# Kernel optimization log

Measured on AMD Instinct MI355X. Metric: run time of the kernel, lower is better.

The kernel has to match this reference:

```python
import jax, jax.numpy as jnp
import numpy as np

DEPTH = 4
HEADS = 8
DIM_HEAD = 32
NUM_CLUSTERS = 64
KMEANS_ITERS = 10
EPS = 1e-5


def layer_norm(x, g, b):
    m = jnp.mean(x, axis=-1, keepdims=True)
    v = jnp.var(x, axis=-1, keepdims=True)
    return (x - m) * jax.lax.rsqrt(v + EPS) * g + b


def kmeans_cluster(xf, k, iters):
    # xf: [P, D]. Lloyd's algorithm with deterministic init (first k points).
    centers = xf[:k]
    x_sq = jnp.sum(xf * xf, axis=-1, keepdims=True)  # [P,1]

    def assign(c):
        # squared distances [P, K]
        d = x_sq - 2.0 * (xf @ c.T) + jnp.sum(c * c, axis=-1)[None, :]
        return jnp.argmin(d, axis=-1)

    def step(c, _):
        labels = assign(c)
        sums = jax.ops.segment_sum(xf, labels, num_segments=k)
        counts = jax.ops.segment_sum(jnp.ones((xf.shape[0],), xf.dtype), labels, num_segments=k)
        new_c = jnp.where(counts[:, None] > 0, sums / jnp.maximum(counts, 1.0)[:, None], c)
        return new_c, None

    centers, _ = jax.lax.scan(step, centers, None, length=iters)
    labels = assign(centers)
    return centers[labels]  # gather: [P, D]


def setup_inputs() -> dict:
    key = jax.random.key(0)
    ks = jax.random.split(key, 8)
    B, N, D, L, M = 8, 1024, 256, DEPTH, 1024
    s = 0.02
    return {
        "x": jax.random.normal(ks[0], (B, N, D), jnp.float32),
        "ln1_g": jnp.ones((L, D), jnp.float32),
        "ln1_b": jnp.zeros((L, D), jnp.float32),
        "Wq": jax.random.normal(ks[1], (L, D, HEADS * DIM_HEAD), jnp.float32) * s,
        "Wkv": jax.random.normal(ks[2], (L, D, 2 * HEADS * DIM_HEAD), jnp.float32) * s,
        "Wo": jax.random.normal(ks[3], (L, HEADS * DIM_HEAD, D), jnp.float32) * s,
        "bo": jnp.zeros((L, D), jnp.float32),
        "ln2_g": jnp.ones((L, D), jnp.float32),
        "ln2_b": jnp.zeros((L, D), jnp.float32),
        "W1": jax.random.normal(ks[4], (L, D, M), jnp.float32) * s,
        "b1": jnp.zeros((L, M), jnp.float32),
        "W2": jax.random.normal(ks[5], (L, M, D), jnp.float32) * s,
        "b2": jnp.zeros((L, D), jnp.float32),
        "kW": jax.random.normal(ks[6], (D, D), jnp.float32) * s,
        "kb": jnp.zeros((D,), jnp.float32),
    }


def reference(x, ln1_g, ln1_b, Wq, Wkv, Wo, bo, ln2_g, ln2_b, W1, b1, W2, b2, kW, kb):
    B, N, D = x.shape
    h, dh = HEADS, DIM_HEAD
    scale = dh ** -0.5
    for l in range(DEPTH):
        # PreNorm self-attention + residual
        xn = layer_norm(x, ln1_g[l], ln1_b[l])
        q = (xn @ Wq[l]).reshape(B, N, h, dh)
        kv = xn @ Wkv[l]
        k, v = jnp.split(kv, 2, axis=-1)
        k = k.reshape(B, N, h, dh)
        v = v.reshape(B, N, h, dh)
        dots = jnp.einsum("bqhd,bkhd->bhqk", q, k) * scale
        attn = jax.nn.softmax(dots, axis=-1)
        out = jnp.einsum("bhqk,bkhd->bqhd", attn, v).reshape(B, N, h * dh)
        x = out @ Wo[l] + bo[l] + x
        # PreNorm FFN + residual
        xn = layer_norm(x, ln2_g[l], ln2_b[l])
        hdd = jax.nn.gelu(xn @ W1[l] + b1[l], approximate=False)
        x = hdd @ W2[l] + b2[l] + x
    # KMeans module: cluster flattened tokens, gather centers, linear transform.
    xf = x.reshape(B * N, D)
    clustered = kmeans_cluster(xf, NUM_CLUSTERS, KMEANS_ITERS)
    clustered = jax.lax.stop_gradient(clustered)  # torch detaches before sklearn
    clustered = clustered.reshape(B, N, D)
    return clustered @ kW + kb
```

## Files before the change

### kernel.cpp

```cpp
#include <hip/hip_runtime.h>
#include <hip/hip_bf16.h>
#include <math.h>

#define BN 8192
#define DMODEL 256
#define FFN 1024
#define NCLUST 64

typedef unsigned short u16;
typedef unsigned int u32;
typedef __attribute__((ext_vector_type(8))) short s16x8;
typedef __attribute__((ext_vector_type(8))) unsigned short u16x8;
typedef __attribute__((ext_vector_type(4))) unsigned short u16x4;
typedef __attribute__((ext_vector_type(4))) float f32x4;

__device__ __forceinline__ float bf2f(u16 v) {
    union { unsigned int u; float f; } w; w.u = ((unsigned int)v) << 16; return w.f;
}
__device__ __forceinline__ u16 f2bf(float f) {
    union { float f; unsigned int u; } w; w.f = f;
    unsigned int r = w.u + 0x7fffu + ((w.u >> 16) & 1u);
    return (u16)(r >> 16);
}

__device__ __forceinline__ void gl16(const u16* g, u16* l) {
    __builtin_amdgcn_global_load_lds((const __attribute__((address_space(1))) u32*)g,
                                     (__attribute__((address_space(3))) u32*)l, 16, 0, 0);
}

#define BARRIER_LGKM() asm volatile("s_waitcnt lgkmcnt(0)\n\ts_barrier" ::: "memory")
#define MEMFENCE_ORDER() asm volatile("" ::: "memory")

__device__ __forceinline__ int sw32(int row, int col) { return row * 32 + (col ^ (((row >> 1) & 3) << 3)); }
__device__ __forceinline__ int sw64(int row, int col) { return row * 64 + (col ^ ((row & 7) << 3)); }

__global__ __launch_bounds__(256) void ln_wave(const float* __restrict__ x, const float* __restrict__ g,
                                               const float* __restrict__ b, u16* __restrict__ yh,
                                               u16* __restrict__ yl) {
    int t = threadIdx.x, w = t >> 6, l = t & 63;
    int row = blockIdx.x * 4 + w;
    const float* xr = x + (size_t)row * DMODEL;
    float4 v = *reinterpret_cast<const float4*>(xr + l * 4);
    float s = v.x + v.y + v.z + v.w;
    for (int off = 1; off < 64; off <<= 1) s += __shfl_xor(s, off);
    float mean = s * (1.0f / 256.0f);
    float4 dv = make_float4(v.x - mean, v.y - mean, v.z - mean, v.w - mean);
    float vs = dv.x * dv.x + dv.y * dv.y + dv.z * dv.z + dv.w * dv.w;
    for (int off = 1; off < 64; off <<= 1) vs += __shfl_xor(vs, off);
    float rs = rsqrtf(vs * (1.0f / 256.0f) + 1e-5f);
    float4 gg = *reinterpret_cast<const float4*>(g + l * 4);
    float4 bb = *reinterpret_cast<const float4*>(b + l * 4);
    float os[4] = {dv.x * rs * gg.x + bb.x, dv.y * rs * gg.y + bb.y,
                   dv.z * rs * gg.z + bb.z, dv.w * rs * gg.w + bb.w};
    u16x4 hv, lv;
#pragma unroll
    for (int j = 0; j < 4; j++) { u16 hh = f2bf(os[j]); hv[j] = hh; lv[j] = f2bf(os[j] - bf2f(hh)); }
    size_t o = (size_t)row * DMODEL + l * 4;
    *reinterpret_cast<u16x4*>(yh + o) = hv;
    *reinterpret_cast<u16x4*>(yl + o) = lv;
}

__device__ __forceinline__ void wconv_body(const float* __restrict__ W, u16* __restrict__ th,
                                           u16* __restrict__ tl, int K, int N, int bx, int by) {
    __shared__ float T[64][65];
    int k0 = by * 64, n0 = bx * 64;
    int t = threadIdx.x;
    int r = t >> 4, c4 = (t & 15) * 4;
#pragma unroll
    for (int i = 0; i < 4; i++) {
        float4 x = *reinterpret_cast<const float4*>(W + (size_t)(k0 + r + 16 * i) * N + n0 + c4);
        T[r + 16 * i][c4] = x.x; T[r + 16 * i][c4 + 1] = x.y;
        T[r + 16 * i][c4 + 2] = x.z; T[r + 16 * i][c4 + 3] = x.w;
    }
    __syncthreads();
#pragma unroll
    for (int i = 0; i < 4; i++) {
        int n = r + 16 * i;
        u16x4 h4, l4;
#pragma unroll
        for (int j = 0; j < 4; j++) {
            float v = T[c4 + j][n];
            u16 h = f2bf(v);
            h4[j] = h; l4[j] = f2bf(v - bf2f(h));
        }
        *reinterpret_cast<u16x4*>(th + (size_t)(n0 + n) * K + k0 + c4) = h4;
        *reinterpret_cast<u16x4*>(tl + (size_t)(n0 + n) * K + k0 + c4) = l4;
    }
}

__global__ __launch_bounds__(256) void wconv_all(const float* __restrict__ Wq, const float* __restrict__ Wkv,
                                                 const float* __restrict__ Wo, const float* __restrict__ W1,
                                                 const float* __restrict__ W2,
                                                 u16* __restrict__ wqkvh, u16* __restrict__ wqkvl,
                                                 u16* __restrict__ woh, u16* __restrict__ wol,
                                                 u16* __restrict__ w1h, u16* __restrict__ w1l,
                                                 u16* __restrict__ w2h, u16* __restrict__ w2l) {
    int f = blockIdx.x;
    if (f < 16)       wconv_body(Wq,  wqkvh,               wqkvl,               256, 256,  f & 3,  f >> 2);
    else if (f < 48)  { int g = f - 16;  wconv_body(Wkv, wqkvh + 65536,       wqkvl + 65536,       256, 512,  g & 7,  g >> 3); }
    else if (f < 64)  { int g = f - 48;  wconv_body(Wo,  woh,                 wol,                 256, 256,  g & 3,  g >> 2); }
    else if (f < 128) { int g = f - 64;  wconv_body(W1,  w1h,                 w1l,                 256, 1024, g & 15, g >> 4); }
    else              { int g = f - 128; wconv_body(W2,  w2h,                 w2l,                 1024, 256, g & 3,  g >> 2); }
}

template<int BM, int BNT>
__global__ __launch_bounds__(256) void gemm_t(const u16* __restrict__ Ath, const u16* __restrict__ Atl,
                                              const u16* __restrict__ Bth, const u16* __restrict__ Btl,
                                              const float* __restrict__ bias, const float* __restrict__ resid,
                                              float* __restrict__ Cf, u16* __restrict__ Ch, u16* __restrict__ Cl,
                                              int M, int N, int K, int fuse_gelu) {
    __shared__ u16 Ah[2][BM * 32], Al[2][BM * 32];
    __shared__ u16 Bh[2][BNT * 32], Bl[2][BNT * 32];
    constexpr int WAVES_N = (BM == 128 && BNT == 64) ? 1 : 2;
    constexpr int WAVES_M = 4 / WAVES_N;
    constexpr int MI = BM / (16 * WAVES_M);
    constexpr int NI = BNT / (16 * WAVES_N);
    constexpr int SEGS = (BM + BNT) / 32;
    constexpr int ASEG = BM / 16, BSEG = BNT / 16;
    int t = threadIdx.x;
    int m0 = blockIdx.y * BM, n0 = blockIdx.x * BNT;
    int L = t & 63, w = t >> 6, fr = L & 15, quad = L >> 4;
    int wm = (WAVES_N == 1) ? w : (w & 1);
    int wn = (WAVES_N == 1) ? 0 : (w >> 1);

    const u16* gsrc[SEGS];
    u16* ldst[SEGS];
    u32 dlt[SEGS];
    {
        int lr = L >> 2, lc = (L & 3) * 8;
#pragma unroll
        for (int i = 0; i < SEGS; i++) {
            int s = w * SEGS + i;
            const u16* gb; u16* lb; int r; u32 d;
            if (s < ASEG)                 { gb = Ath + (size_t)m0 * K; lb = &Ah[0][0]; r = s * 16;                 d = BM * 32; }
            else if (s < 2 * ASEG)        { gb = Atl + (size_t)m0 * K; lb = &Al[0][0]; r = (s - ASEG) * 16;        d = BM * 32; }
            else if (s < 2 * ASEG + BSEG) { gb = Bth + (size_t)n0 * K; lb = &Bh[0][0]; r = (s - 2 * ASEG) * 16;    d = BNT * 32; }
            else                          { gb = Btl + (size_t)n0 * K; lb = &Bl[0][0]; r = (s - 2 * ASEG - BSEG) * 16; d = BNT * 32; }
            int row = r + lr;
            int scol = lc ^ (((row >> 1) & 3) << 3);
            gsrc[i] = gb + (size_t)row * K + scol;
            ldst[i] = lb + r * 32;
            dlt[i] = d;
        }
    }

    f32x4 acc[MI][NI];
#pragma unroll
    for (int i = 0; i < MI; i++)
#pragma unroll
        for (int j = 0; j < NI; j++) acc[i][j] = (f32x4){0.0f, 0.0f, 0.0f, 0.0f};

    const int NT = K >> 5;
#pragma unroll
    for (int i = 0; i < SEGS; i++) gl16(gsrc[i], ldst[i]);

    for (int tt = 0; tt < NT; tt++) {
        asm volatile("s_waitcnt lgkmcnt(0)" ::: "memory");
        __builtin_amdgcn_s_barrier();
        if (tt + 1 < NT) {
            int k0n = (tt + 1) * 32;
            u32 sel = (u32)((tt + 1) & 1);
#pragma unroll
            for (int i = 0; i < SEGS; i++) gl16(gsrc[i] + k0n, ldst[i] + sel * dlt[i]);
            asm volatile("s_waitcnt vmcnt(%0)" :: "n"(SEGS) : "memory");
        } else {
            asm volatile("s_waitcnt vmcnt(0)" ::: "memory");
        }
        __builtin_amdgcn_s_barrier();
        __builtin_amdgcn_sched_barrier(0);
        int cb = tt & 1;
        const u16* AhB = &Ah[cb][0]; const u16* AlB = &Al[cb][0];
        const u16* BhB = &Bh[cb][0]; const u16* BlB = &Bl[cb][0];
        s16x8 ah[MI], al[MI];
#pragma unroll
        for (int mi = 0; mi < MI; mi++) {
            int row = wm * (MI * 16) + mi * 16 + fr;
            ah[mi] = *reinterpret_cast<const s16x8*>(&AhB[sw32(row, quad * 8)]);
            al[mi] = *reinterpret_cast<const s16x8*>(&AlB[sw32(row, quad * 8)]);
        }
        __builtin_amdgcn_s_setprio(1);
#pragma unroll
        for (int ni = 0; ni < NI; ni++) {
            int rn = wn * (NI * 16) + ni * 16 + fr;
            s16x8 bhf = *reinterpret_cast<const s16x8*>(&BhB[sw32(rn, quad * 8)]);
            s16x8 blf = *reinterpret_cast<const s16x8*>(&BlB[sw32(rn, quad * 8)]);
#pragma unroll
            for (int mi = 0; mi < MI; mi++) {
                acc[mi][ni] = __builtin_amdgcn_mfma_f32_16x16x32_bf16(ah[mi], bhf, acc[mi][ni], 0, 0, 0);
                acc[mi][ni] = __builtin_amdgcn_mfma_f32_16x16x32_bf16(ah[mi], blf, acc[mi][ni], 0, 0, 0);
                acc[mi][ni] = __builtin_amdgcn_mfma_f32_16x16x32_bf16(al[mi], bhf, acc[mi][ni], 0, 0, 0);
            }
        }
        __builtin_amdgcn_s_setprio(0);
    }
#pragma unroll
    for (int mi = 0; mi < MI; mi++) {
#pragma unroll
        for (int ni = 0; ni < NI; ni++) {
#pragma unroll
            for (int r = 0; r < 4; r++) {
                int row = m0 + wm * (MI * 16) + mi * 16 + quad * 4 + r;
                int col = n0 + wn * (NI * 16) + ni * 16 + fr;
                float v = acc[mi][ni][r];
                if (bias) v += bias[col];
                if (fuse_gelu) v = 0.5f * v * (1.0f + erff(v * 0.70710678118654752f));
                if (resid) v += resid[(size_t)row * N + col];
                size_t o = (size_t)row * N + col;
                if (Cf) Cf[o] = v;
                if (Ch) { u16 hh = f2bf(v); Ch[o] = hh; Cl[o] = f2bf(v - bf2f(hh)); }
            }
        }
    }
}

__global__ __launch_bounds__(256) void attn12(const u16* __restrict__ qkvh, const u16* __restrict__ qkvl,
                                              u16* __restrict__ aoh, u16* __restrict__ aol) {
    int bh = blockIdx.x, b = bh >> 3, h = bh & 7;
    int qt = blockIdx.y;
    int t = threadIdx.x, L = t & 63, w = t >> 6;
    int fr = L & 15, quad = L >> 4;
    __shared__ u16 KH[2][64 * 32], KL[2][64 * 32];
    __shared__ u16 VTH[32 * 64], VTL[32 * 64];
    __shared__ u16 PH[4][16 * 64], PL[4][16 * 64];
    const float scale = 0.17677669529663687f;
    const int ROWS = 768;

    const u16* ksrc[2];
    u16* kdst[2];
    {
        int lr = L >> 2, lc = (L & 3) * 8;
#pragma unroll
        for (int i = 0; i < 2; i++) {
            int s = w * 2 + i;
            const u16* gb = (s < 4) ? qkvh : qkvl;
            u16* lb = (s < 4) ? &KH[0][0] : &KL[0][0];
            int r = (s & 3) * 16;
            int row = r + lr;
            int scol = lc ^ (((row >> 1) & 3) << 3);
            ksrc[i] = gb + ((size_t)(b * 1024) + row) * ROWS + 256 + h * 32 + scol;
            kdst[i] = lb + r * 32;
        }
    }

    size_t qoff = (size_t)(b * 1024 + qt * 64 + w * 16 + fr) * ROWS + h * 32 + quad * 8;
    s16x8 aqh = *reinterpret_cast<const s16x8*>(qkvh + qoff);
    s16x8 aql = *reinterpret_cast<const s16x8*>(qkvl + qoff);

    int vp = t >> 3, vd0 = (t & 7) * 4;
    const u16* vh_ptr = qkvh + (size_t)(b * 1024 + 2 * vp) * ROWS + 512 + h * 32 + vd0;
    const u16* vl_ptr = qkvl + (size_t)(b * 1024 + 2 * vp) * ROWS + 512 + h * 32 + vd0;
    u16x4 vh0, vh1, vl0, vl1;
#define LOADV(kt_) do { size_t o_ = (size_t)((kt_) * 64) * ROWS;                                  \
        vh0 = *reinterpret_cast<const u16x4*>(vh_ptr + o_);                                       \
        vh1 = *reinterpret_cast<const u16x4*>(vh_ptr + o_ + ROWS);                                \
        vl0 = *reinterpret_cast<const u16x4*>(vl_ptr + o_);                                       \
        vl1 = *reinterpret_cast<const u16x4*>(vl_ptr + o_ + ROWS); } while (0)

    gl16(ksrc[0], kdst[0]);
    gl16(ksrc[1], kdst[1]);
    MEMFENCE_ORDER();
    LOADV(0);

    float m_i = -1e30f, l_i = 0.0f;
    f32x4 acc_o[2];
    acc_o[0] = (f32x4){0.0f, 0.0f, 0.0f, 0.0f};
    acc_o[1] = (f32x4){0.0f, 0.0f, 0.0f, 0.0f};

#pragma unroll 2
    for (int kt = 0; kt < 16; kt++) {
        int cur = kt & 1;
        BARRIER_LGKM();
        if (kt < 15) {
            size_t koff = (size_t)((kt + 1) * 64) * ROWS;
            u32 sel = (u32)((kt + 1) & 1) * (64 * 32);
            gl16(ksrc[0] + koff, kdst[0] + sel);
            gl16(ksrc[1] + koff, kdst[1] + sel);
        }
        {
#pragma unroll
            for (int i = 0; i < 4; i++) {
                int idx = sw64(vd0 + i, 2 * vp);
                *reinterpret_cast<u32*>(&VTH[idx]) = (u32)vh0[i] | ((u32)vh1[i] << 16);
                *reinterpret_cast<u32*>(&VTL[idx]) = (u32)vl0[i] | ((u32)vl1[i] << 16);
            }
        }
        BARRIER_LGKM();
        f32x4 sv[4];
        __builtin_amdgcn_s_setprio(1);
#pragma unroll
        for (int ni = 0; ni < 4; ni++) {
            s16x8 bkh = *reinterpret_cast<s16x8*>(&KH[cur][sw32(ni * 16 + fr, quad * 8)]);
            s16x8 bkl = *reinterpret_cast<s16x8*>(&KL[cur][sw32(ni * 16 + fr, quad * 8)]);
            f32x4 c = (f32x4){0.0f, 0.0f, 0.0f, 0.0f};
            c = __builtin_amdgcn_mfma_f32_16x16x32_bf16(bkh, aqh, c, 0, 0, 0);
            c = __builtin_amdgcn_mfma_f32_16x16x32_bf16(bkl, aqh, c, 0, 0, 0);
            c = __builtin_amdgcn_mfma_f32_16x16x32_bf16(bkh, aql, c, 0, 0, 0);
            sv[ni] = c;
        }
        __builtin_amdgcn_s_setprio(0);
        if (kt < 15) LOADV(kt + 1);
        float p[16];
        float ml = -1e30f;
#pragma unroll
        for (int ni = 0; ni < 4; ni++)
#pragma unroll
            for (int r = 0; r < 4; r++) { float v = sv[ni][r] * scale; p[ni * 4 + r] = v; ml = fmaxf(ml, v); }
        ml = fmaxf(ml, __shfl_xor(ml, 16));
        ml = fmaxf(ml, __shfl_xor(ml, 32));
        float mnew = fmaxf(m_i, ml);
        float alpha = __expf(m_i - mnew);
        m_i = mnew;
        float rs = 0.0f;
#pragma unroll
        for (int i = 0; i < 16; i++) { float e = __expf(p[i] - mnew); p[i] = e; rs += e; }
        rs += __shfl_xor(rs, 16);
        rs += __shfl_xor(rs, 32);
        l_i = l_i * alpha + rs;
#pragma unroll
        for (int ni = 0; ni < 4; ni++) {
            float p0 = p[ni * 4], p1 = p[ni * 4 + 1], p2 = p[ni * 4 + 2], p3 = p[ni * 4 + 3];
            u16 h0 = f2bf(p0), h1 = f2bf(p1), h2 = f2bf(p2), h3 = f2bf(p3);
            u16 e0 = f2bf(p0 - bf2f(h0)), e1 = f2bf(p1 - bf2f(h1));
            u16 e2 = f2bf(p2 - bf2f(h2)), e3 = f2bf(p3 - bf2f(h3));
            int c0 = sw64(fr, ni * 16 + quad * 4);
            int c1 = sw64(fr, ni * 16 + quad * 4 + 2);
            *reinterpret_cast<u32*>(&PH[w][c0]) = (u32)h0 | ((u32)h1 << 16);
            *reinterpret_cast<u32*>(&PH[w][c1]) = (u32)h2 | ((u32)h3 << 16);
            *reinterpret_cast<u32*>(&PL[w][c0]) = (u32)e0 | ((u32)e1 << 16);
            *reinterpret_cast<u32*>(&PL[w][c1]) = (u32)e2 | ((u32)e3 << 16);
        }
        float a4[4];
#pragma unroll
        for (int r = 0; r < 4; r++) a4[r] = __shfl(alpha, quad * 4 + r);
        acc_o[0][0] *= a4[0]; acc_o[0][1] *= a4[1]; acc_o[0][2] *= a4[2]; acc_o[0][3] *= a4[3];
        acc_o[1][0] *= a4[0]; acc_o[1][1] *= a4[1]; acc_o[1][2] *= a4[2]; acc_o[1][3] *= a4[3];
        __builtin_amdgcn_s_setprio(1);
#pragma unroll
        for (int ks = 0; ks < 2; ks++) {
            s16x8 aph = *reinterpret_cast<s16x8*>(&PH[w][sw64(fr, ks * 32 + quad * 8)]);
            s16x8 apl = *reinterpret_cast<s16x8*>(&PL[w][sw64(fr, ks * 32 + quad * 8)]);
#pragma unroll
            for (int ns = 0; ns < 2; ns++) {
                s16x8 bvh = *reinterpret_cast<s16x8*>(&VTH[sw64(ns * 16 + fr, ks * 32 + quad * 8)]);
                s16x8 bvl = *reinterpret_cast<s16x8*>(&VTL[sw64(ns * 16 + fr, ks * 32 + quad * 8)]);
                acc_o[ns] = __builtin_amdgcn_mfma_f32_16x16x32_bf16(aph, bvh, acc_o[ns], 0, 0, 0);
                acc_o[ns] = __builtin_amdgcn_mfma_f32_16x16x32_bf16(aph, bvl, acc_o[ns], 0, 0, 0);
                acc_o[ns] = __builtin_amdgcn_mfma_f32_16x16x32_bf16(apl, bvh, acc_o[ns], 0, 0, 0);
            }
        }
        __builtin_amdgcn_s_setprio(0);
    }
#undef LOADV
    float invl = 1.0f / l_i;
#pragma unroll
    for (int r = 0; r < 4; r++) {
        float iv = __shfl(invl, quad * 4 + r);
        size_t rowbase = ((size_t)(b * 1024 + qt * 64 + w * 16 + quad * 4 + r)) * DMODEL + h * 32;
        float v0 = acc_o[0][r] * iv, v1 = acc_o[1][r] * iv;
        u16 h0 = f2bf(v0); aoh[rowbase + fr] = h0;      aol[rowbase + fr] = f2bf(v0 - bf2f(h0));
        u16 h1 = f2bf(v1); aoh[rowbase + 16 + fr] = h1; aol[rowbase + 16 + fr] = f2bf(v1 - bf2f(h1));
    }
}

__global__ __launch_bounds__(64) void csq_k(const float* __restrict__ centers, float* __restrict__ csq) {
    int j = blockIdx.x, l = threadIdx.x;
    float4 c4 = *reinterpret_cast<const float4*>(centers + j * DMODEL + l * 4);
    float s = c4.x * c4.x + c4.y * c4.y + c4.z * c4.z + c4.w * c4.w;
    for (int off = 1; off < 64; off <<= 1) s += __shfl_xor(s, off);
    if (l == 0) csq[j] = s;
}

__global__ __launch_bounds__(256) void km_distmin(const float* __restrict__ A, const float* __restrict__ Cn,
                                                  const float* __restrict__ csq, int* __restrict__ labels) {
    __shared__ float As[16][34];
    __shared__ float Bs[16][64];
    int t = threadIdx.x, tx = t & 15, ty = t >> 4;
    int m0 = blockIdx.x * 32;
    int mr = t & 31, kq = (t >> 5) * 2;
    int jb = t & 63, kb = (t >> 6) * 4;
    float acc[2][4] = {};
    for (int k0 = 0; k0 < 256; k0 += 16) {
        __syncthreads();
        {
            float2 a2 = *reinterpret_cast<const float2*>(A + (size_t)(m0 + mr) * DMODEL + k0 + kq);
            As[kq][mr] = a2.x; As[kq + 1][mr] = a2.y;
        }
        {
            float4 c4 = *reinterpret_cast<const float4*>(Cn + (size_t)jb * DMODEL + k0 + kb);
            Bs[kb][jb] = c4.x; Bs[kb + 1][jb] = c4.y; Bs[kb + 2][jb] = c4.z; Bs[kb + 3][jb] = c4.w;
        }
        __syncthreads();
#pragma unroll
        for (int kk = 0; kk < 16; kk++) {
            float2 a2v = *reinterpret_cast<float2*>(&As[kk][ty * 2]);
            float4 b4 = *reinterpret_cast<float4*>(&Bs[kk][tx * 4]);
            float a[2] = {a2v.x, a2v.y};
            float bf[4] = {b4.x, b4.y, b4.z, b4.w};
#pragma unroll
            for (int i = 0; i < 2; i++)
#pragma unroll
                for (int j = 0; j < 4; j++) acc[i][j] += a[i] * bf[j];
        }
    }
    float4 cs4 = *reinterpret_cast<const float4*>(csq + tx * 4);
    float csv[4] = {cs4.x, cs4.y, cs4.z, cs4.w};
#pragma unroll
    for (int i = 0; i < 2; i++) {
        float best = csv[0] - 2.0f * acc[i][0]; int bi = tx * 4;
#pragma unroll
        for (int j = 1; j < 4; j++) {
            float v = csv[j] - 2.0f * acc[i][j];
            if (v < best) { best = v; bi = tx * 4 + j; }
        }
        for (int off = 1; off < 16; off <<= 1) {
            float ov = __shfl_xor(best, off);
            int oi = __shfl_xor(bi, off);
            if (ov < best || (ov == best && oi < bi)) { best = ov; bi = oi; }
        }
        if (tx == 0) labels[m0 + ty * 2 + i] = bi;
    }
}

__global__ __launch_bounds__(256) void km_segsum(const int* __restrict__ labels, const float* __restrict__ xf,
                                                 float* __restrict__ sums16, float* __restrict__ counts16) {
    int c = blockIdx.x, j = blockIdx.y, t = threadIdx.x;
    __shared__ int labs[512];
    if (t < 128) {
        int4 l4 = *reinterpret_cast<const int4*>(labels + c * 512 + t * 4);
        labs[t * 4] = l4.x; labs[t * 4 + 1] = l4.y; labs[t * 4 + 2] = l4.z; labs[t * 4 + 3] = l4.w;
    }
    __syncthreads();
    float acc = 0.0f, cnt = 0.0f;
    const float* xb = xf + (size_t)c * 512 * DMODEL;
    for (int i = 0; i < 512; i++) {
        if (labs[i] == j) { acc += xb[(size_t)i * DMODEL + t]; cnt += 1.0f; }
    }
    sums16[((size_t)c * NCLUST + j) * DMODEL + t] = acc;
    if (t == 0) counts16[c * NCLUST + j] = cnt;
}

__global__ __launch_bounds__(256) void km_update(float* __restrict__ centers, const float* __restrict__ sums16,
                                                 const float* __restrict__ counts16, float* __restrict__ csq) {
    __shared__ float red[256];
    int j = blockIdx.x, d = threadIdx.x;
    float c = 0.0f;
#pragma unroll
    for (int cc = 0; cc < 16; cc++) c += counts16[cc * NCLUST + j];
    float sv = 0.0f;
#pragma unroll
    for (int cc = 0; cc < 16; cc++) sv += sums16[((size_t)cc * NCLUST + j) * DMODEL + d];
    float cv = centers[j * DMODEL + d];
    if (c > 0.0f) cv = sv / fmaxf(c, 1.0f);
    centers[j * DMODEL + d] = cv;
    red[d] = cv * cv;
    __syncthreads();
    for (int off = 128; off; off >>= 1) { if (d < off) red[d] += red[d + off]; __syncthreads(); }
    if (d == 0) csq[j] = red[0];
}

__global__ __launch_bounds__(256) void nproj(const float* __restrict__ centers, const float* __restrict__ kW,
                                             const float* __restrict__ kb2, float* __restrict__ outc) {
    int idx = blockIdx.x * 256 + threadIdx.x;
    if (idx >= NCLUST * DMODEL) return;
    int row = idx >> 8, col = idx & 255;
    const float* cr = centers + row * DMODEL;
    float acc = 0.0f;
    for (int d = 0; d < DMODEL; d++) acc += cr[d] * kW[(size_t)d * DMODEL + col];
    outc[idx] = acc + kb2[col];
}

__global__ __launch_bounds__(256) void km_gather(const int* __restrict__ labels, const float* __restrict__ outc,
                                                 float* __restrict__ out) {
    int i = blockIdx.x, t = threadIdx.x;
    int lab = labels[i];
    out[(size_t)i * DMODEL + t] = outc[lab * DMODEL + t];
}

extern "C" void kernel_launch(void* const* d_in, const int* in_sizes, int n_in,
                              void* d_out, int out_size, void* d_ws, size_t ws_size,
                              hipStream_t stream) {
    const float* x_in  = (const float*)d_in[0];
    const float* ln1_g = (const float*)d_in[1];
    const float* ln1_b = (const float*)d_in[2];
    const float* Wq    = (const float*)d_in[3];
    const float* Wkv   = (const float*)d_in[4];
    const float* Wo    = (const float*)d_in[5];
    const float* bo    = (const float*)d_in[6];
    const float* ln2_g = (const float*)d_in[7];
    const float* ln2_b = (const float*)d_in[8];
    const float* W1    = (const float*)d_in[9];
    const float* b1    = (const float*)d_in[10];
    const float* W2    = (const float*)d_in[11];
    const float* b2    = (const float*)d_in[12];
    const float* kWp   = (const float*)d_in[13];
    const float* kbp   = (const float*)d_in[14];
    float* out = (float*)d_out;

    const size_t NEEDED = 53477376;
    if (ws_size < NEEDED) {
        hipMemsetAsync(d_out, 0, (size_t)out_size * sizeof(float), stream);
        return;
    }

    char* ws = (char*)d_ws;
    float* xf      = (float*)(ws);
    u16*   xnh     = (u16*)  (ws + 8388608);
    u16*   xnl     = (u16*)  (ws + 12582912);
    u16*   aoh     = xnh;
    u16*   aol     = xnl;
    u16*   qkvh    = (u16*)  (ws + 16777216);
    u16*   qkvl    = (u16*)  (ws + 29360128);
    u16*   hbh     = (u16*)  (ws + 16777216);
    u16*   hbl     = (u16*)  (ws + 33554432);
    float* centers = (float*)(ws + 41943040);
    float* csqb    = (float*)(ws + 42008576);
    float* counts16= (float*)(ws + 42008832);
    int*   labels  = (int*)  (ws + 42012928);
    float* outc    = (float*)(ws + 42045696);
    float* sums16  = (float*)(ws + 42111232);
    u16*   wr      = (u16*)  (ws + 50331648);
    u16 *wqkvh = wr,          *wqkvl = wr + 196608;
    u16 *woh = wr + 393216,   *wol = wr + 458752;
    u16 *w1h = wr + 524288,   *w1l = wr + 786432;
    u16 *w2h = wr + 1048576,  *w2l = wr + 1310720;

    hipMemcpyAsync(xf, x_in, (size_t)BN * DMODEL * sizeof(float), hipMemcpyDeviceToDevice, stream);

    for (int l = 0; l < 4; l++) {
        wconv_all<<<192, 256, 0, stream>>>(Wq + (size_t)l * 65536, Wkv + (size_t)l * 131072,
                                           Wo + (size_t)l * 65536, W1 + (size_t)l * 262144,
                                           W2 + (size_t)l * 262144,
                                           wqkvh, wqkvl, woh, wol, w1h, w1l, w2h, w2l);

        ln_wave<<<BN / 4, 256, 0, stream>>>(xf, ln1_g + l * 256, ln1_b + l * 256, xnh, xnl);
        gemm_t<128, 128><<<dim3(6, 64), 256, 0, stream>>>(xnh, xnl, wqkvh, wqkvl, nullptr, nullptr,
                                                          nullptr, qkvh, qkvl, BN, 768, 256, 0);
        attn12<<<dim3(64, 16), 256, 0, stream>>>(qkvh, qkvl, aoh, aol);
        gemm_t<64, 64><<<dim3(4, 128), 256, 0, stream>>>(aoh, aol, woh, wol, bo + l * 256, xf,
                                                         xf, nullptr, nullptr, BN, 256, 256, 0);
        ln_wave<<<BN / 4, 256, 0, stream>>>(xf, ln2_g + l * 256, ln2_b + l * 256, xnh, xnl);
        gemm_t<128, 128><<<dim3(8, 64), 256, 0, stream>>>(xnh, xnl, w1h, w1l, b1 + l * 1024, nullptr,
                                                          nullptr, hbh, hbl, BN, 1024, 256, 1);
        gemm_t<64, 64><<<dim3(4, 128), 256, 0, stream>>>(hbh, hbl, w2h, w2l, b2 + l * 256, xf,
                                                         xf, nullptr, nullptr, BN, 256, 1024, 0);
    }

    hipMemcpyAsync(centers, xf, NCLUST * DMODEL * sizeof(float), hipMemcpyDeviceToDevice, stream);
    csq_k<<<64, 64, 0, stream>>>(centers, csqb);
    for (int it = 0; it < 10; it++) {
        km_distmin<<<256, 256, 0, stream>>>(xf, centers, csqb, labels);
        km_segsum<<<dim3(16, NCLUST), 256, 0, stream>>>(labels, xf, sums16, counts16);
        km_update<<<64, 256, 0, stream>>>(centers, sums16, counts16, csqb);
    }
    km_distmin<<<256, 256, 0, stream>>>(xf, centers, csqb, labels);
    nproj<<<64, 256, 0, stream>>>(centers, kWp, kbp, outc);
    km_gather<<<BN, 256, 0, stream>>>(labels, outc, out);
}
```

Before: 1.332 ms.

## Bucket-sort labels in k-means segsum and use packed bf16 conversion in attention

The k-means segment-sum no longer has each block scan all 512 labels per cluster. It now splits tokens into 64 chunks of 128, builds per-chunk counting-sort offsets and a permutation in shared memory, and sums only the rows belonging to each cluster. The update kernel then reduces over 64 partials and skips empty ones. Separately, the attention kernel's hi/lo bf16 split of P uses the v_cvt_pk_bf16_f32 instruction instead of manual rounding. The serial single-thread histogram and the O(128^2) rank loop add some latency, and the hardware conversion may round slightly differently than the manual round-to-nearest-even code.

Measured after the change: 1.432 ms. 7.5% more time.

```diff
diff --git a/kernel.cpp b/kernel.cpp
--- a/kernel.cpp
+++ b/kernel.cpp
@@ -22,6 +22,12 @@
     unsigned int r = w.u + 0x7fffu + ((w.u >> 16) & 1u);
     return (u16)(r >> 16);
 }
+__device__ __forceinline__ u32 cvtpk(float lo, float hi) {
+    u32 r;
+    asm("v_cvt_pk_bf16_f32 %0, %1, %2" : "=v"(r) : "v"(lo), "v"(hi));
+    return r;
+}
+__device__ __forceinline__ float u2f(u32 u) { union { u32 u; float f; } w; w.u = u; return w.f; }
 
 __device__ __forceinline__ void gl16(const u16* g, u16* l) {
     __builtin_amdgcn_global_load_lds((const __attribute__((address_space(1))) u32*)g,
@@ -213,7 +219,7 @@
     }
 }
 
-__global__ __launch_bounds__(256) void attn12(const u16* __restrict__ qkvh, const u16* __restrict__ qkvl,
+__global__ __launch_bounds__(256) void attn13(const u16* __restrict__ qkvh, const u16* __restrict__ qkvl,
                                               u16* __restrict__ aoh, u16* __restrict__ aol) {
     int bh = blockIdx.x, b = bh >> 3, h = bh & 7;
     int qt = blockIdx.y;
@@ -319,15 +325,18 @@
 #pragma unroll
         for (int ni = 0; ni < 4; ni++) {
             float p0 = p[ni * 4], p1 = p[ni * 4 + 1], p2 = p[ni * 4 + 2], p3 = p[ni * 4 + 3];
-            u16 h0 = f2bf(p0), h1 = f2bf(p1), h2 = f2bf(p2), h3 = f2bf(p3);
-            u16 e0 = f2bf(p0 - bf2f(h0)), e1 = f2bf(p1 - bf2f(h1));
-            u16 e2 = f2bf(p2 - bf2f(h2)), e3 = f2bf(p3 - bf2f(h3));
+            u32 qh01 = cvtpk(p0, p1), qh23 = cvtpk(p2, p3);
+            float e0 = p0 - u2f(qh01 << 16);
+            float e1 = p1 - u2f(qh01 & 0xffff0000u);
+            float e2 = p2 - u2f(qh23 << 16);
+            float e3 = p3 - u2f(qh23 & 0xffff0000u);
+            u32 ql01 = cvtpk(e0, e1), ql23 = cvtpk(e2, e3);
             int c0 = sw64(fr, ni * 16 + quad * 4);
             int c1 = sw64(fr, ni * 16 + quad * 4 + 2);
-            *reinterpret_cast<u32*>(&PH[w][c0]) = (u32)h0 | ((u32)h1 << 16);
-            *reinterpret_cast<u32*>(&PH[w][c1]) = (u32)h2 | ((u32)h3 << 16);
-            *reinterpret_cast<u32*>(&PL[w][c0]) = (u32)e0 | ((u32)e1 << 16);
-            *reinterpret_cast<u32*>(&PL[w][c1]) = (u32)e2 | ((u32)e3 << 16);
+            *reinterpret_cast<u32*>(&PH[w][c0]) = qh01;
+            *reinterpret_cast<u32*>(&PH[w][c1]) = qh23;
+            *reinterpret_cast<u32*>(&PL[w][c0]) = ql01;
+            *reinterpret_cast<u32*>(&PL[w][c1]) = ql23;
         }
         float a4[4];
 #pragma unroll
@@ -422,33 +431,52 @@
 }
 
 __global__ __launch_bounds__(256) void km_segsum(const int* __restrict__ labels, const float* __restrict__ xf,
-                                                 float* __restrict__ sums16, float* __restrict__ counts16) {
-    int c = blockIdx.x, j = blockIdx.y, t = threadIdx.x;
-    __shared__ int labs[512];
+                                                 float* __restrict__ sums64, float* __restrict__ counts64) {
+    int c = blockIdx.x, g = blockIdx.y, t = threadIdx.x;
+    __shared__ int labs[128];
+    __shared__ int cnt[NCLUST];
+    __shared__ int offs[NCLUST];
+    __shared__ int perm[128];
+    if (t < 128) labs[t] = labels[c * 128 + t];
+    __syncthreads();
+    if (t == 0) {
+        int tmp[1];
+        (void)tmp;
+        for (int j = 0; j < NCLUST; j++) cnt[j] = 0;
+        for (int i = 0; i < 128; i++) cnt[labs[i]]++;
+        int s = 0;
+        for (int j = 0; j < NCLUST; j++) { offs[j] = s; s += cnt[j]; }
+    }
+    __syncthreads();
     if (t < 128) {
-        int4 l4 = *reinterpret_cast<const int4*>(labels + c * 512 + t * 4);
-        labs[t * 4] = l4.x; labs[t * 4 + 1] = l4.y; labs[t * 4 + 2] = l4.z; labs[t * 4 + 3] = l4.w;
+        int lab = labs[t];
+        int r = offs[lab];
+        for (int i = 0; i < 128; i++) r += (i < t && labs[i] == lab) ? 1 : 0;
+        perm[r] = t;
     }
     __syncthreads();
-    float acc = 0.0f, cnt = 0.0f;
-    const float* xb = xf + (size_t)c * 512 * DMODEL;
-    for (int i = 0; i < 512; i++) {
-        if (labs[i] == j) { acc += xb[(size_t)i * DMODEL + t]; cnt += 1.0f; }
-    }
-    sums16[((size_t)c * NCLUST + j) * DMODEL + t] = acc;
-    if (t == 0) counts16[c * NCLUST + j] = cnt;
-}
-
-__global__ __launch_bounds__(256) void km_update(float* __restrict__ centers, const float* __restrict__ sums16,
-                                                 const float* __restrict__ counts16, float* __restrict__ csq) {
+    const float* xb = xf + (size_t)c * 128 * DMODEL;
+    for (int j = g * 16; j < g * 16 + 16; j++) {
+        int n = cnt[j];
+        if (t == 0) counts64[c * NCLUST + j] = (float)n;
+        if (n == 0) continue;
+        float acc = 0.0f;
+        int s0 = offs[j];
+        for (int idx = s0; idx < s0 + n; idx++)
+            acc += xb[(size_t)perm[idx] * DMODEL + t];
+        sums64[((size_t)c * NCLUST + j) * DMODEL + t] = acc;
+    }
+}
+
+__global__ __launch_bounds__(256) void km_update(float* __restrict__ centers, const float* __restrict__ sums64,
+                                                 const float* __restrict__ counts64, float* __restrict__ csq) {
     __shared__ float red[256];
     int j = blockIdx.x, d = threadIdx.x;
-    float c = 0.0f;
-#pragma unroll
-    for (int cc = 0; cc < 16; cc++) c += counts16[cc * NCLUST + j];
-    float sv = 0.0f;
-#pragma unroll
-    for (int cc = 0; cc < 16; cc++) sv += sums16[((size_t)cc * NCLUST + j) * DMODEL + d];
+    float c = 0.0f, sv = 0.0f;
+    for (int cc = 0; cc < 64; cc++) {
+        float n = counts64[cc * NCLUST + j];
+        if (n > 0.0f) { c += n; sv += sums64[((size_t)cc * NCLUST + j) * DMODEL + d]; }
+    }
     float cv = centers[j * DMODEL + d];
     if (c > 0.0f) cv = sv / fmaxf(c, 1.0f);
     centers[j * DMODEL + d] = cv;
@@ -514,10 +542,10 @@
     u16*   hbl     = (u16*)  (ws + 33554432);
     float* centers = (float*)(ws + 41943040);
     float* csqb    = (float*)(ws + 42008576);
-    float* counts16= (float*)(ws + 42008832);
-    int*   labels  = (int*)  (ws + 42012928);
-    float* outc    = (float*)(ws + 42045696);
-    float* sums16  = (float*)(ws + 42111232);
+    float* counts64= (float*)(ws + 42008832);
+    int*   labels  = (int*)  (ws + 42025216);
+    float* outc    = (float*)(ws + 42057984);
+    float* sums64  = (float*)(ws + 42123520);
     u16*   wr      = (u16*)  (ws + 50331648);
     u16 *wqkvh = wr,          *wqkvl = wr + 196608;
     u16 *woh = wr + 393216,   *wol = wr + 458752;
@@ -535,7 +563,7 @@
         ln_wave<<<BN / 4, 256, 0, stream>>>(xf, ln1_g + l * 256, ln1_b + l * 256, xnh, xnl);
         gemm_t<128, 128><<<dim3(6, 64), 256, 0, stream>>>(xnh, xnl, wqkvh, wqkvl, nullptr, nullptr,
                                                           nullptr, qkvh, qkvl, BN, 768, 256, 0);
-        attn12<<<dim3(64, 16), 256, 0, stream>>>(qkvh, qkvl, aoh, aol);
+        attn13<<<dim3(64, 16), 256, 0, stream>>>(qkvh, qkvl, aoh, aol);
         gemm_t<64, 64><<<dim3(4, 128), 256, 0, stream>>>(aoh, aol, woh, wol, bo + l * 256, xf,
                                                          xf, nullptr, nullptr, BN, 256, 256, 0);
         ln_wave<<<BN / 4, 256, 0, stream>>>(xf, ln2_g + l * 256, ln2_b + l * 256, xnh, xnl);
@@ -549,8 +577,8 @@
     csq_k<<<64, 64, 0, stream>>>(centers, csqb);
     for (int it = 0; it < 10; it++) {
         km_distmin<<<256, 256, 0, stream>>>(xf, centers, csqb, labels);
-        km_segsum<<<dim3(16, NCLUST), 256, 0, stream>>>(labels, xf, sums16, counts16);
-        km_update<<<64, 256, 0, stream>>>(centers, sums16, counts16, csqb);
+        km_segsum<<<dim3(64, 4), 256, 0, stream>>>(labels, xf, sums64, counts64);
+        km_update<<<64, 256, 0, stream>>>(centers, sums64, counts64, csqb);
     }
     km_distmin<<<256, 256, 0, stream>>>(xf, centers, csqb, labels);
     nproj<<<64, 256, 0, stream>>>(centers, kWp, kbp, outc);
```
